# Kernel tuning notes

Measured on AMD Instinct MI355X. Metric: run time of the kernel, lower is better.

## Reference

```python
import jax, jax.numpy as jnp
import numpy as np

N_NODES = 50000
N_EDGES = 800000
IN_CH, HID_CH, OUT_CH = 128, 128, 64


def setup_inputs() -> dict:
    key = jax.random.key(0)
    ks = jax.random.split(key, 8)
    x = jax.random.normal(ks[0], (N_NODES, IN_CH), dtype=jnp.float32)
    edge_index = jax.random.randint(ks[1], (2, N_EDGES), 0, N_NODES, dtype=jnp.int64)
    # PyG SAGEConv params: lin_l (applied to aggregated neighbors, has bias),
    # lin_r (applied to root node, no bias). Stored here as [in, out] matrices.
    s1 = 1.0 / np.sqrt(IN_CH)
    s2 = 1.0 / np.sqrt(HID_CH)
    W1l = jax.random.uniform(ks[2], (IN_CH, HID_CH), jnp.float32, -s1, s1)
    b1 = jnp.zeros((HID_CH,), jnp.float32)
    W1r = jax.random.uniform(ks[3], (IN_CH, HID_CH), jnp.float32, -s1, s1)
    W2l = jax.random.uniform(ks[4], (HID_CH, OUT_CH), jnp.float32, -s2, s2)
    b2 = jnp.zeros((OUT_CH,), jnp.float32)
    W2r = jax.random.uniform(ks[5], (HID_CH, OUT_CH), jnp.float32, -s2, s2)
    return {"x": x, "edge_index": edge_index, "W1l": W1l, "b1": b1,
            "W1r": W1r, "W2l": W2l, "b2": b2, "W2r": W2r}


def _sage_conv(x, src, dst, Wl, b, Wr):
    # mean-aggregate source features onto targets, then linear transform
    msg = x[src]                                        # [E, d] gather
    agg = jax.ops.segment_sum(msg, dst, num_segments=N_NODES)   # [N, d]
    deg = jax.ops.segment_sum(jnp.ones((src.shape[0],), x.dtype), dst,
                              num_segments=N_NODES)     # [N]
    mean = agg / jnp.maximum(deg, 1.0)[:, None]
    return mean @ Wl + b + x @ Wr


def reference(x, edge_index, W1l, b1, W1r, W2l, b2, W2r):
    src, dst = edge_index[0], edge_index[1]
    h = jax.nn.relu(_sage_conv(x, src, dst, W1l, b1, W1r))
    # F.dropout(p=0.3) is identity in eval mode
    return _sage_conv(h, src, dst, W2l, b2, W2r)
```

## Files before the change

### kernel.cpp

```cpp
#include <hip/hip_runtime.h>
#include <hip/hip_bf16.h>


#define TBLOCK 256
#define MAXBUCK 256
#define HGRID 512

typedef __attribute__((ext_vector_type(8))) short short8;
typedef __attribute__((ext_vector_type(4))) float f32x4;

__device__ __forceinline__ float bf2f(ushort u) {
    union { unsigned int i; float f; } v;
    v.i = (unsigned int)u << 16;
    return v.f;
}
__device__ __forceinline__ ushort f2bf(float f) {
    union { float f; unsigned int u; } v;
    v.f = f;
    unsigned int r = v.u + 0x7fffu + ((v.u >> 16) & 1u);
    return (ushort)(r >> 16);
}

__device__ __forceinline__ int block_detect_is64(const int* __restrict__ edges) {
    __shared__ int sbad[4];
    int tid = threadIdx.x;
    int bad = 0;
    for (int i = tid; i < 2048; i += TBLOCK)
        if (edges[2 * i + 1] != 0) bad = 1;
    unsigned long long b = __ballot(bad);
    if ((tid & 63) == 0) sbad[tid >> 6] = (b != 0) ? 1 : 0;
    __syncthreads();
    int flag = (sbad[0] | sbad[1] | sbad[2] | sbad[3]) ? 0 : 1;
    __syncthreads();
    return flag;
}

__device__ __forceinline__ int load_src(const int* e, long long i, int E, int is64) {
    return is64 ? e[2 * i] : e[i];
}
__device__ __forceinline__ int load_dst(const int* e, long long i, int E, int is64) {
    return is64 ? e[2 * (long long)E + 2 * i] : e[(long long)E + i];
}

__device__ __forceinline__ void scan_total(const int* __restrict__ total, int NBUCK,
                                           int* __restrict__ s) {
    int t = threadIdx.x;
    s[t] = (t < NBUCK) ? total[t] : 0;
    __syncthreads();
    for (int off = 1; off < TBLOCK; off <<= 1) {
        int xv = (t >= off) ? s[t - off] : 0;
        __syncthreads();
        s[t] += xv;
        __syncthreads();
    }
}

__global__ __launch_bounds__(TBLOCK) void histprep_k(
    const float* __restrict__ x,
    const float* __restrict__ W1l, const float* __restrict__ W1r,
    const float* __restrict__ W2l, const float* __restrict__ W2r,
    const int* __restrict__ edges, int E, int NBUCK,
    ushort* __restrict__ xb, ushort* __restrict__ wc1, ushort* __restrict__ wc2,
    int* __restrict__ counts, int n8, int nxb) {
    __shared__ int lh[MAXBUCK];
    const int b = blockIdx.x;
    const int t = threadIdx.x;
    if (b < HGRID) {
        const int is64 = block_detect_is64(edges);
        for (int i = t; i < NBUCK; i += TBLOCK) lh[i] = 0;
        __syncthreads();
        const int per = (E + HGRID - 1) / HGRID;
        const int b0 = b * per, b1 = min(E, b0 + per);
        for (int i = b0 + t; i < b1; i += TBLOCK)
            atomicAdd(&lh[load_dst(edges, i, E, is64) >> 8], 1);
        __syncthreads();
        for (int j = t; j < NBUCK; j += TBLOCK)
            counts[j * HGRID + b] = lh[j];
    } else {
        int pb = b - HGRID;
        if (pb < nxb) {
            int i = pb * TBLOCK + t;
            if (i >= n8) return;
            const float4* p = (const float4*)x + (size_t)i * 2;
            float4 a = p[0], bb = p[1];
            short8 o;
            o[0] = f2bf(a.x); o[1] = f2bf(a.y); o[2] = f2bf(a.z); o[3] = f2bf(a.w);
            o[4] = f2bf(bb.x); o[5] = f2bf(bb.y); o[6] = f2bf(bb.z); o[7] = f2bf(bb.w);
            *(short8*)(xb + (size_t)i * 8) = o;
        } else {
            int i = (pb - nxb) * TBLOCK + t;
            if (i < 32768) {
                int j = i & 7;
                int rest = i >> 3;
                int n = rest & 127;
                int k = ((rest >> 7) << 3) | j;
                float w = (k < 128) ? W1l[k * 128 + n] : W1r[(k - 128) * 128 + n];
                wc1[i] = f2bf(w);
            } else if (i < 49152) {
                int i2 = i - 32768;
                int j = i2 & 7;
                int rest = i2 >> 3;
                int n = rest & 127;
                int k = ((rest >> 7) << 3) | j;
                float w = (n < 64) ? W2l[k * 64 + n] : W2r[k * 64 + (n - 64)];
                wc2[i2] = f2bf(w);
            }
        }
    }
}

__global__ __launch_bounds__(TBLOCK) void scanA_k(int* __restrict__ counts,
                                                  int* __restrict__ total) {
    __shared__ int s[TBLOCK];
    const int j = blockIdx.x;
    const int t = threadIdx.x;
    int* row = counts + (size_t)j * HGRID;
    int v0 = row[2 * t];
    int v1 = row[2 * t + 1];
    s[t] = v0 + v1;
    __syncthreads();
    for (int off = 1; off < TBLOCK; off <<= 1) {
        int xv = (t >= off) ? s[t - off] : 0;
        __syncthreads();
        s[t] += xv;
        __syncthreads();
    }
    int excl = (t == 0) ? 0 : s[t - 1];
    row[2 * t] = excl;
    row[2 * t + 1] = excl + v0;
    if (t == TBLOCK - 1) total[j] = s[t];
}

__global__ __launch_bounds__(TBLOCK) void scatterA_k(const int* __restrict__ edges, int E,
                                                     const int* __restrict__ counts,
                                                     const int* __restrict__ total,
                                                     unsigned int* __restrict__ packed,
                                                     int NBUCK) {
    const int is64 = block_detect_is64(edges);
    __shared__ int s[TBLOCK];
    __shared__ int lb[MAXBUCK];
    __shared__ int lh[MAXBUCK];
    const int b = blockIdx.x;
    const int t = threadIdx.x;
    scan_total(total, NBUCK, s);
    if (t < NBUCK) {
        int excl = (t == 0) ? 0 : s[t - 1];
        lb[t] = excl + counts[t * HGRID + b];
        lh[t] = 0;
    }
    __syncthreads();
    const int per = (E + HGRID - 1) / HGRID;
    const int b0 = b * per, b1 = min(E, b0 + per);
    for (int i = b0 + t; i < b1; i += TBLOCK) {
        int sv = load_src(edges, i, E, is64);
        int d = load_dst(edges, i, E, is64);
        int bk = d >> 8;
        int pos = lb[bk] + atomicAdd(&lh[bk], 1);
        packed[pos] = (unsigned int)sv | ((unsigned int)(d & 255) << 24);
    }
}

__global__ __launch_bounds__(TBLOCK) void buildB_k(const unsigned int* __restrict__ packed,
                                                   const int* __restrict__ total,
                                                   int* __restrict__ offs,
                                                   int* __restrict__ degi,
                                                   float* __restrict__ invdeg,
                                                   int* __restrict__ csr, int N, int NBUCK) {
    __shared__ int s[TBLOCK];
    __shared__ int cnt[TBLOCK], scn[TBLOCK], cur[TBLOCK];
    int t = threadIdx.x;
    int bucket = blockIdx.x;
    scan_total(total, NBUCK, s);
    int e0 = (bucket == 0) ? 0 : s[bucket - 1];
    int e1 = s[bucket];
    cnt[t] = 0;
    cur[t] = 0;
    __syncthreads();
    for (int i = e0 + t; i < e1; i += TBLOCK)
        atomicAdd(&cnt[packed[i] >> 24], 1);
    __syncthreads();
    scn[t] = cnt[t];
    __syncthreads();
    for (int off = 1; off < TBLOCK; off <<= 1) {
        int x = (t >= off) ? scn[t - off] : 0;
        __syncthreads();
        scn[t] += x;
        __syncthreads();
    }
    int excl = (t == 0) ? 0 : scn[t - 1];
    int node = bucket * 256 + t;
    if (node < N) {
        offs[node] = e0 + excl;
        degi[node] = cnt[t];
        invdeg[node] = 1.0f / fmaxf((float)cnt[t], 1.0f);
    }
    __syncthreads();
    cnt[t] = excl;
    __syncthreads();
    for (int i = e0 + t; i < e1; i += TBLOCK) {
        unsigned int p = packed[i];
        int nl = p >> 24;
        int pos = e0 + cnt[nl] + atomicAdd(&cur[nl], 1);
        csr[pos] = (int)(p & 0xFFFFFFu);
    }
}

template <int C, bool ACCUM>
__global__ __launch_bounds__(TBLOCK) void gatherb_k(const ushort* __restrict__ feat,
                                                    const int* __restrict__ csr,
                                                    const int* __restrict__ offs,
                                                    const int* __restrict__ degi,
                                                    const float* __restrict__ invdeg,
                                                    ushort* __restrict__ outB,
                                                    float* __restrict__ outF, int N) {
    constexpr int G = C / 8;
    constexpr int NPB = TBLOCK / G;
    int n = blockIdx.x * NPB + threadIdx.x / G;
    if (n >= N) return;
    int lane = threadIdx.x % G;
    int c = lane * 8;
    int s0 = offs[n];
    int d = degi[n];
    float acc[8] = {0.f, 0.f, 0.f, 0.f, 0.f, 0.f, 0.f, 0.f};
    for (int base = 0; base < d; base += G) {
        int rem = d - base;
        int my = (lane < rem) ? csr[s0 + base + lane] : 0;
        if (rem >= G) {
#pragma unroll
            for (int j = 0; j < G; j++) {
                int s = __shfl(my, j, G);
                short8 v = *(const short8*)(feat + (size_t)s * C + c);
#pragma unroll
                for (int q = 0; q < 8; q++) acc[q] += bf2f((ushort)v[q]);
            }
        } else {
            for (int j = 0; j < rem; j++) {
                int s = __shfl(my, j, G);
                short8 v = *(const short8*)(feat + (size_t)s * C + c);
#pragma unroll
                for (int q = 0; q < 8; q++) acc[q] += bf2f((ushort)v[q]);
            }
        }
    }
    float sc = invdeg[n];
    if (ACCUM) {
        float* o = outF + (size_t)n * C + c;
        float4 p0 = *(float4*)o;
        float4 p1 = *(float4*)(o + 4);
        p0.x += sc * acc[0]; p0.y += sc * acc[1]; p0.z += sc * acc[2]; p0.w += sc * acc[3];
        p1.x += sc * acc[4]; p1.y += sc * acc[5]; p1.z += sc * acc[6]; p1.w += sc * acc[7];
        *(float4*)o = p0;
        *(float4*)(o + 4) = p1;
    } else {
        short8 o;
#pragma unroll
        for (int q = 0; q < 8; q++) o[q] = f2bf(sc * acc[q]);
        *(short8*)(outB + (size_t)n * C + c) = o;
    }
}

__global__ __launch_bounds__(TBLOCK) void gg1_k(const ushort* __restrict__ xb,
                                                const int* __restrict__ csr,
                                                const int* __restrict__ offs,
                                                const int* __restrict__ degi,
                                                const float* __restrict__ invdeg,
                                                const ushort* __restrict__ wc1,
                                                const float* __restrict__ b1,
                                                ushort* __restrict__ hb, int N) {
    __shared__ __align__(16) ushort sW[256 * 128];
    for (int i = threadIdx.x * 8; i < 256 * 128; i += TBLOCK * 8)
        *(short8*)&sW[i] = *(const short8*)&wc1[i];

    const int wave = threadIdx.x >> 6;
    const int lane = threadIdx.x & 63;
    const int quad = lane >> 4;
    const int l16 = lane & 15;
    const int m0 = blockIdx.x * 128 + wave * 32;
    const int cq = quad * 8;

    short8 aagg[2][4];
#pragma unroll
    for (int t = 0; t < 2; t++) {
        int m = m0 + t * 16 + l16;
        if (m > N - 1) m = N - 1;
        int s0 = offs[m];
        int d = degi[m];
        float ga[4][8];
#pragma unroll
        for (int c = 0; c < 4; c++)
#pragma unroll
            for (int q = 0; q < 8; q++) ga[c][q] = 0.f;
        for (int e = 0; e < d; e++) {
            int s = csr[s0 + e];
            const ushort* row = xb + (size_t)s * 128 + cq;
            short8 v0 = *(const short8*)(row);
            short8 v1 = *(const short8*)(row + 32);
            short8 v2 = *(const short8*)(row + 64);
            short8 v3 = *(const short8*)(row + 96);
#pragma unroll
            for (int q = 0; q < 8; q++) {
                ga[0][q] += bf2f((ushort)v0[q]);
                ga[1][q] += bf2f((ushort)v1[q]);
                ga[2][q] += bf2f((ushort)v2[q]);
                ga[3][q] += bf2f((ushort)v3[q]);
            }
        }
        float iv = invdeg[m];
#pragma unroll
        for (int c = 0; c < 4; c++)
#pragma unroll
            for (int q = 0; q < 8; q++) aagg[t][c][q] = f2bf(ga[c][q] * iv);
    }
    __syncthreads();

    f32x4 acc[2][8];
#pragma unroll
    for (int t = 0; t < 2; t++)
#pragma unroll
        for (int nt = 0; nt < 8; nt++) acc[t][nt] = (f32x4){0.f, 0.f, 0.f, 0.f};

#pragma unroll
    for (int kb = 0; kb < 128; kb += 32) {
        int c = kb >> 5;
        int k = kb + cq;
#pragma unroll
        for (int nt = 0; nt < 8; nt++) {
            short8 b = *(const short8*)&sW[((k >> 3) * 128 + nt * 16 + l16) * 8];
            acc[0][nt] = __builtin_amdgcn_mfma_f32_16x16x32_bf16(aagg[0][c], b, acc[0][nt], 0, 0, 0);
            acc[1][nt] = __builtin_amdgcn_mfma_f32_16x16x32_bf16(aagg[1][c], b, acc[1][nt], 0, 0, 0);
        }
    }
#pragma unroll
    for (int kb = 128; kb < 256; kb += 32) {
        int k = kb + cq;
        short8 a[2];
#pragma unroll
        for (int t = 0; t < 2; t++) {
            int m = m0 + t * 16 + l16;
            if (m > N - 1) m = N - 1;
            a[t] = *(const short8*)(xb + (size_t)m * 128 + (k - 128));
        }
#pragma unroll
        for (int nt = 0; nt < 8; nt++) {
            short8 b = *(const short8*)&sW[((k >> 3) * 128 + nt * 16 + l16) * 8];
            acc[0][nt] = __builtin_amdgcn_mfma_f32_16x16x32_bf16(a[0], b, acc[0][nt], 0, 0, 0);
            acc[1][nt] = __builtin_amdgcn_mfma_f32_16x16x32_bf16(a[1], b, acc[1][nt], 0, 0, 0);
        }
    }

#pragma unroll
    for (int t = 0; t < 2; t++)
#pragma unroll
        for (int r = 0; r < 4; r++) {
            int m = m0 + t * 16 + quad * 4 + r;
            if (m >= N) continue;
#pragma unroll
            for (int nt = 0; nt < 8; nt++) {
                int n = nt * 16 + l16;
                float v = fmaxf(acc[t][nt][r] + b1[n], 0.f);
                hb[(size_t)m * 128 + n] = f2bf(v);
            }
        }
}

__global__ __launch_bounds__(TBLOCK) void gemm2_k(const ushort* __restrict__ A0,
                                                  const ushort* __restrict__ wc,
                                                  const float* __restrict__ bias,
                                                  ushort* __restrict__ outB,
                                                  float* __restrict__ outF, int N) {
    constexpr int KTOT = 128;
    __shared__ __align__(16) ushort sW[KTOT * 128];
    for (int i = threadIdx.x * 8; i < KTOT * 128; i += TBLOCK * 8)
        *(short8*)&sW[i] = *(const short8*)&wc[i];
    __syncthreads();

    const int wave = threadIdx.x >> 6;
    const int lane = threadIdx.x & 63;
    const int quad = lane >> 4;
    const int l16 = lane & 15;
    const int m0 = (blockIdx.x * 4 + wave) * 32;
    if (m0 >= N) return;

    f32x4 acc[2][8];
#pragma unroll
    for (int t = 0; t < 2; t++)
#pragma unroll
        for (int nt = 0; nt < 8; nt++) acc[t][nt] = (f32x4){0.f, 0.f, 0.f, 0.f};

    const int k0q = quad * 8;
#pragma unroll
    for (int kb = 0; kb < KTOT; kb += 32) {
        int k = kb + k0q;
        short8 a[2];
#pragma unroll
        for (int t = 0; t < 2; t++) {
            int m = m0 + t * 16 + l16;
            if (m > N - 1) m = N - 1;
            a[t] = *(const short8*)(A0 + (size_t)m * 128 + k);
        }
#pragma unroll
        for (int nt = 0; nt < 8; nt++) {
            short8 b = *(const short8*)&sW[((k >> 3) * 128 + nt * 16 + l16) * 8];
            acc[0][nt] = __builtin_amdgcn_mfma_f32_16x16x32_bf16(a[0], b, acc[0][nt], 0, 0, 0);
            acc[1][nt] = __builtin_amdgcn_mfma_f32_16x16x32_bf16(a[1], b, acc[1][nt], 0, 0, 0);
        }
    }

#pragma unroll
    for (int t = 0; t < 2; t++) {
#pragma unroll
        for (int r = 0; r < 4; r++) {
            int m = m0 + t * 16 + quad * 4 + r;
            if (m >= N) continue;
#pragma unroll
            for (int nt = 0; nt < 8; nt++) {
                int n = nt * 16 + l16;
                float v = acc[t][nt][r];
                if (n < 64) outB[(size_t)m * 64 + n] = f2bf(v);
                else outF[(size_t)m * 64 + (n - 64)] = v + bias[n - 64];
            }
        }
    }
}

extern "C" void kernel_launch(void* const* d_in, const int* in_sizes, int n_in,
                              void* d_out, int out_size, void* d_ws, size_t ws_size,
                              hipStream_t stream) {
    const float* x = (const float*)d_in[0];
    const int* edges = (const int*)d_in[1];
    const float* W1l = (const float*)d_in[2];
    const float* b1 = (const float*)d_in[3];
    const float* W1r = (const float*)d_in[4];
    const float* W2l = (const float*)d_in[5];
    const float* b2 = (const float*)d_in[6];
    const float* W2r = (const float*)d_in[7];
    float* out = (float*)d_out;

    const int N = in_sizes[0] / 128;
    const int E = in_sizes[1] / 2;
    const int Na = (N + 63) & ~63;
    const int NBUCK = (N + 255) >> 8;
    const int n8 = N * 128 / 8;
    const int nxb = (n8 + TBLOCK - 1) / TBLOCK;

    char* WS = (char*)d_ws;
    size_t off = 0;
    auto alloc = [&](size_t bytes) {
        void* p = WS + off;
        off = (off + bytes + 255) & ~(size_t)255;
        return p;
    };
    int* counts = (int*)alloc((size_t)MAXBUCK * HGRID * 4);
    int* total = (int*)alloc((size_t)MAXBUCK * 4);
    int* offs = (int*)alloc((size_t)Na * 4);
    int* degi = (int*)alloc((size_t)Na * 4);
    float* invdeg = (float*)alloc((size_t)Na * 4);
    unsigned int* packed = (unsigned int*)alloc((size_t)E * 4);
    int* csr = (int*)alloc((size_t)E * 4);
    ushort* xb = (ushort*)alloc((size_t)N * 128 * 2);
    ushort* hb = (ushort*)alloc((size_t)N * 128 * 2);
    ushort* t2b = (ushort*)alloc((size_t)N * 64 * 2);
    ushort* wc1 = (ushort*)alloc(32768 * 2);
    ushort* wc2 = (ushort*)alloc(16384 * 2);

    histprep_k<<<HGRID + nxb + 192, TBLOCK, 0, stream>>>(
        x, W1l, W1r, W2l, W2r, edges, E, NBUCK, xb, wc1, wc2, counts, n8, nxb);
    scanA_k<<<NBUCK, TBLOCK, 0, stream>>>(counts, total);
    scatterA_k<<<HGRID, TBLOCK, 0, stream>>>(edges, E, counts, total, packed, NBUCK);
    buildB_k<<<NBUCK, TBLOCK, 0, stream>>>(packed, total, offs, degi, invdeg, csr, N, NBUCK);

    gg1_k<<<(N + 127) / 128, TBLOCK, 0, stream>>>(
        xb, csr, offs, degi, invdeg, wc1, b1, hb, N);

    gemm2_k<<<(N + 127) / 128, TBLOCK, 0, stream>>>(
        hb, wc2, b2, t2b, out, N);
    gatherb_k<64, true><<<(N + 31) / 32, TBLOCK, 0, stream>>>(
        t2b, csr, offs, degi, invdeg, nullptr, out, N);
}
```

Baseline: 211.9 us.

## Overlap root GEMM with edge scatter and split layer-1 gather from GEMM

Layer 1's root transform (x @ W1r + b1) moves into extra blocks of the scatter kernel, so it runs while the CSR is still being built, and writes a partial result into hb. The fused gather+GEMM kernel is split in two. A standalone gatherb kernel writes the mean-aggregated features to a new bf16 buffer, and a smaller GEMM kernel then adds the neighbour term, reads back hb and applies ReLU. This aims to improve occupancy and latency hiding in the irregular gather, and to hide the root GEMM behind scatter work. In exchange it adds an extra global write and read of a 128-wide bf16 buffer, one more launch, and an extra bf16 rounding of the partial sum.

```diff
diff --git a/kernel.cpp b/kernel.cpp
--- a/kernel.cpp
+++ b/kernel.cpp
@@ -131,32 +131,83 @@
     if (t == TBLOCK - 1) total[j] = s[t];
 }
 
-__global__ __launch_bounds__(TBLOCK) void scatterA_k(const int* __restrict__ edges, int E,
-                                                     const int* __restrict__ counts,
-                                                     const int* __restrict__ total,
-                                                     unsigned int* __restrict__ packed,
-                                                     int NBUCK) {
-    const int is64 = block_detect_is64(edges);
+__global__ __launch_bounds__(TBLOCK) void scatroot_k(
+    const int* __restrict__ edges, int E,
+    const int* __restrict__ counts, const int* __restrict__ total,
+    unsigned int* __restrict__ packed, int NBUCK,
+    const ushort* __restrict__ xb, const ushort* __restrict__ wc1,
+    const float* __restrict__ b1, ushort* __restrict__ hb, int N, int RB) {
+    __shared__ __align__(16) ushort sW[128 * 128];
     __shared__ int s[TBLOCK];
     __shared__ int lb[MAXBUCK];
     __shared__ int lh[MAXBUCK];
-    const int b = blockIdx.x;
     const int t = threadIdx.x;
-    scan_total(total, NBUCK, s);
-    if (t < NBUCK) {
-        int excl = (t == 0) ? 0 : s[t - 1];
-        lb[t] = excl + counts[t * HGRID + b];
-        lh[t] = 0;
-    }
-    __syncthreads();
-    const int per = (E + HGRID - 1) / HGRID;
-    const int b0 = b * per, b1 = min(E, b0 + per);
-    for (int i = b0 + t; i < b1; i += TBLOCK) {
-        int sv = load_src(edges, i, E, is64);
-        int d = load_dst(edges, i, E, is64);
-        int bk = d >> 8;
-        int pos = lb[bk] + atomicAdd(&lh[bk], 1);
-        packed[pos] = (unsigned int)sv | ((unsigned int)(d & 255) << 24);
+
+    if ((int)blockIdx.x < RB) {
+        const ushort* wroot = wc1 + 16384;
+        for (int i = t * 8; i < 128 * 128; i += TBLOCK * 8)
+            *(short8*)&sW[i] = *(const short8*)&wroot[i];
+        __syncthreads();
+        const int wave = t >> 6;
+        const int lane = t & 63;
+        const int quad = lane >> 4;
+        const int l16 = lane & 15;
+        const int m0 = (blockIdx.x * 4 + wave) * 32;
+        if (m0 >= N) return;
+        f32x4 acc[2][8];
+#pragma unroll
+        for (int tt = 0; tt < 2; tt++)
+#pragma unroll
+            for (int nt = 0; nt < 8; nt++) acc[tt][nt] = (f32x4){0.f, 0.f, 0.f, 0.f};
+        const int k0q = quad * 8;
+#pragma unroll
+        for (int kb = 0; kb < 128; kb += 32) {
+            int k = kb + k0q;
+            short8 a[2];
+#pragma unroll
+            for (int tt = 0; tt < 2; tt++) {
+                int m = m0 + tt * 16 + l16;
+                if (m > N - 1) m = N - 1;
+                a[tt] = *(const short8*)(xb + (size_t)m * 128 + k);
+            }
+#pragma unroll
+            for (int nt = 0; nt < 8; nt++) {
+                short8 b = *(const short8*)&sW[((k >> 3) * 128 + nt * 16 + l16) * 8];
+                acc[0][nt] = __builtin_amdgcn_mfma_f32_16x16x32_bf16(a[0], b, acc[0][nt], 0, 0, 0);
+                acc[1][nt] = __builtin_amdgcn_mfma_f32_16x16x32_bf16(a[1], b, acc[1][nt], 0, 0, 0);
+            }
+        }
+#pragma unroll
+        for (int tt = 0; tt < 2; tt++)
+#pragma unroll
+            for (int r = 0; r < 4; r++) {
+                int m = m0 + tt * 16 + quad * 4 + r;
+                if (m >= N) continue;
+#pragma unroll
+                for (int nt = 0; nt < 8; nt++) {
+                    int n = nt * 16 + l16;
+                    hb[(size_t)m * 128 + n] = f2bf(acc[tt][nt][r] + b1[n]);
+                }
+            }
+    } else {
+        const int b = blockIdx.x - RB;
+        const int is64 = block_detect_is64(edges);
+        scan_total(total, NBUCK, s);
+        if (t < NBUCK) {
+            int excl = (t == 0) ? 0 : s[t - 1];
+            lb[t] = excl + counts[t * HGRID + b];
+            lh[t] = 0;
+        }
+        __syncthreads();
+        const int per = (E + HGRID - 1) / HGRID;
+        const int b0 = b * per, b1e = min(E, b0 + per);
+        for (int i = b0 + t; i < b1e; i += TBLOCK) {
+            int sv = load_src(edges, i, E, is64);
+            int d = load_dst(edges, i, E, is64);
+            int bk = d >> 8;
+            int pos = lb[bk] + atomicAdd(&lh[bk], 1);
+            packed[pos] = (unsigned int)sv | ((unsigned int)(d & 255) << 24);
+        }
     }
 }
 
@@ -259,59 +310,20 @@
     }
 }
 
-__global__ __launch_bounds__(TBLOCK) void gg1_k(const ushort* __restrict__ xb,
-                                                const int* __restrict__ csr,
-                                                const int* __restrict__ offs,
-                                                const int* __restrict__ degi,
-                                                const float* __restrict__ invdeg,
-                                                const ushort* __restrict__ wc1,
-                                                const float* __restrict__ b1,
-                                                ushort* __restrict__ hb, int N) {
-    __shared__ __align__(16) ushort sW[256 * 128];
-    for (int i = threadIdx.x * 8; i < 256 * 128; i += TBLOCK * 8)
+__global__ __launch_bounds__(TBLOCK) void gemm1b_k(const ushort* __restrict__ agg1b,
+                                                   const ushort* __restrict__ wc1,
+                                                   ushort* __restrict__ hb, int N) {
+    __shared__ __align__(16) ushort sW[128 * 128];
+    for (int i = threadIdx.x * 8; i < 128 * 128; i += TBLOCK * 8)
         *(short8*)&sW[i] = *(const short8*)&wc1[i];
+    __syncthreads();
 
     const int wave = threadIdx.x >> 6;
     const int lane = threadIdx.x & 63;
     const int quad = lane >> 4;
     const int l16 = lane & 15;
-    const int m0 = blockIdx.x * 128 + wave * 32;
-    const int cq = quad * 8;
-
-    short8 aagg[2][4];
-#pragma unroll
-    for (int t = 0; t < 2; t++) {
-        int m = m0 + t * 16 + l16;
-        if (m > N - 1) m = N - 1;
-        int s0 = offs[m];
-        int d = degi[m];
-        float ga[4][8];
-#pragma unroll
-        for (int c = 0; c < 4; c++)
-#pragma unroll
-            for (int q = 0; q < 8; q++) ga[c][q] = 0.f;
-        for (int e = 0; e < d; e++) {
-            int s = csr[s0 + e];
-            const ushort* row = xb + (size_t)s * 128 + cq;
-            short8 v0 = *(const short8*)(row);
-            short8 v1 = *(const short8*)(row + 32);
-            short8 v2 = *(const short8*)(row + 64);
-            short8 v3 = *(const short8*)(row + 96);
-#pragma unroll
-            for (int q = 0; q < 8; q++) {
-                ga[0][q] += bf2f((ushort)v0[q]);
-                ga[1][q] += bf2f((ushort)v1[q]);
-                ga[2][q] += bf2f((ushort)v2[q]);
-                ga[3][q] += bf2f((ushort)v3[q]);
-            }
-        }
-        float iv = invdeg[m];
-#pragma unroll
-        for (int c = 0; c < 4; c++)
-#pragma unroll
-            for (int q = 0; q < 8; q++) aagg[t][c][q] = f2bf(ga[c][q] * iv);
-    }
-    __syncthreads();
+    const int m0 = (blockIdx.x * 4 + wave) * 32;
+    if (m0 >= N) return;
 
     f32x4 acc[2][8];
 #pragma unroll
@@ -319,26 +331,16 @@
 #pragma unroll
         for (int nt = 0; nt < 8; nt++) acc[t][nt] = (f32x4){0.f, 0.f, 0.f, 0.f};
 
+    const int k0q = quad * 8;
 #pragma unroll
     for (int kb = 0; kb < 128; kb += 32) {
-        int c = kb >> 5;
-        int k = kb + cq;
-#pragma unroll
-        for (int nt = 0; nt < 8; nt++) {
-            short8 b = *(const short8*)&sW[((k >> 3) * 128 + nt * 16 + l16) * 8];
-            acc[0][nt] = __builtin_amdgcn_mfma_f32_16x16x32_bf16(aagg[0][c], b, acc[0][nt], 0, 0, 0);
-            acc[1][nt] = __builtin_amdgcn_mfma_f32_16x16x32_bf16(aagg[1][c], b, acc[1][nt], 0, 0, 0);
-        }
-    }
-#pragma unroll
-    for (int kb = 128; kb < 256; kb += 32) {
-        int k = kb + cq;
+        int k = kb + k0q;
         short8 a[2];
 #pragma unroll
         for (int t = 0; t < 2; t++) {
             int m = m0 + t * 16 + l16;
             if (m > N - 1) m = N - 1;
-            a[t] = *(const short8*)(xb + (size_t)m * 128 + (k - 128));
+            a[t] = *(const short8*)(agg1b + (size_t)m * 128 + k);
         }
 #pragma unroll
         for (int nt = 0; nt < 8; nt++) {
@@ -349,7 +351,7 @@
     }
 
 #pragma unroll
-    for (int t = 0; t < 2; t++)
+    for (int t = 0; t < 2; t++) {
 #pragma unroll
         for (int r = 0; r < 4; r++) {
             int m = m0 + t * 16 + quad * 4 + r;
@@ -357,10 +359,11 @@
 #pragma unroll
             for (int nt = 0; nt < 8; nt++) {
                 int n = nt * 16 + l16;
-                float v = fmaxf(acc[t][nt][r] + b1[n], 0.f);
-                hb[(size_t)m * 128 + n] = f2bf(v);
-            }
-        }
+                float v = acc[t][nt][r] + bf2f(hb[(size_t)m * 128 + n]);
+                hb[(size_t)m * 128 + n] = f2bf(fmaxf(v, 0.f));
+            }
+        }
+    }
 }
 
 __global__ __launch_bounds__(TBLOCK) void gemm2_k(const ushort* __restrict__ A0,
@@ -442,6 +445,7 @@
     const int NBUCK = (N + 255) >> 8;
     const int n8 = N * 128 / 8;
     const int nxb = (n8 + TBLOCK - 1) / TBLOCK;
+    const int RB = (N + 127) / 128;
 
     char* WS = (char*)d_ws;
     size_t off = 0;
@@ -458,6 +462,7 @@
     unsigned int* packed = (unsigned int*)alloc((size_t)E * 4);
     int* csr = (int*)alloc((size_t)E * 4);
     ushort* xb = (ushort*)alloc((size_t)N * 128 * 2);
+    ushort* agg1b = (ushort*)alloc((size_t)N * 128 * 2);
     ushort* hb = (ushort*)alloc((size_t)N * 128 * 2);
     ushort* t2b = (ushort*)alloc((size_t)N * 64 * 2);
     ushort* wc1 = (ushort*)alloc(32768 * 2);
@@ -466,11 +471,13 @@
     histprep_k<<<HGRID + nxb + 192, TBLOCK, 0, stream>>>(
         x, W1l, W1r, W2l, W2r, edges, E, NBUCK, xb, wc1, wc2, counts, n8, nxb);
     scanA_k<<<NBUCK, TBLOCK, 0, stream>>>(counts, total);
-    scatterA_k<<<HGRID, TBLOCK, 0, stream>>>(edges, E, counts, total, packed, NBUCK);
+    scatroot_k<<<RB + HGRID, TBLOCK, 0, stream>>>(
+        edges, E, counts, total, packed, NBUCK, xb, wc1, b1, hb, N, RB);
     buildB_k<<<NBUCK, TBLOCK, 0, stream>>>(packed, total, offs, degi, invdeg, csr, N, NBUCK);
 
-    gg1_k<<<(N + 127) / 128, TBLOCK, 0, stream>>>(
-        xb, csr, offs, degi, invdeg, wc1, b1, hb, N);
+    gatherb_k<128, false><<<(N + 15) / 16, TBLOCK, 0, stream>>>(
+        xb, csr, offs, degi, invdeg, agg1b, nullptr, N);
+    gemm1b_k<<<(N + 127) / 128, TBLOCK, 0, stream>>>(agg1b, wc1, hb, N);
 
     gemm2_k<<<(N + 127) / 128, TBLOCK, 0, stream>>>(
         hb, wc2, b2, t2b, out, N);
```

Result: faster. 194.2 us (-8.4%).
